# Kernel tuning notes

Hardware: AMD Instinct MI355X
Metric: run time of the kernel (lower is better)

The kernel has to match this reference:

```python
import jax, jax.numpy as jnp
import numpy as np

NUM_HEADS = 16
EMB_SIZE = 1024
HEAD_SIZE = 64


def setup_inputs() -> dict:
    key = jax.random.key(0)
    ks = jax.random.split(key, 9)
    H, E, D = NUM_HEADS, EMB_SIZE, HEAD_SIZE
    s = 1.0 / np.sqrt(E)
    X = jax.random.normal(ks[0], (4, 2048, E), dtype=jnp.float32)
    Wq = jax.random.uniform(ks[1], (H, E, D), jnp.float32, -s, s)
    Wk = jax.random.uniform(ks[2], (H, E, D), jnp.float32, -s, s)
    Wv = jax.random.uniform(ks[3], (H, E, D), jnp.float32, -s, s)
    bq = jax.random.uniform(ks[4], (H, D), jnp.float32, -s, s)
    bk = jax.random.uniform(ks[5], (H, D), jnp.float32, -s, s)
    bv = jax.random.uniform(ks[6], (H, D), jnp.float32, -s, s)
    so = 1.0 / np.sqrt(H * D)
    Wo = jax.random.uniform(ks[7], (H * D, E), jnp.float32, -so, so)
    bo = jax.random.uniform(ks[8], (E,), jnp.float32, -so, so)
    return {"X": X, "Wq": Wq, "Wk": Wk, "Wv": Wv, "bq": bq, "bk": bk, "bv": bv, "Wo": Wo, "bo": bo}


def reference(X, Wq, Wk, Wv, bq, bk, bv, Wo, bo):
    B, S, E = X.shape
    H, _, D = Wq.shape
    # per-head projections (batched over heads)
    q = jnp.einsum('bse,hed->bhsd', X, Wq) + bq[None, :, None, :]
    k = jnp.einsum('bse,hed->bhsd', X, Wk) + bk[None, :, None, :]
    v = jnp.einsum('bse,hed->bhsd', X, Wv) + bv[None, :, None, :]
    # causal scaled-dot-product attention
    scores = jnp.einsum('bhsd,bhtd->bhst', q, k) / jnp.sqrt(jnp.float32(D))
    causal = jnp.tril(jnp.ones((S, S), dtype=bool))
    scores = jnp.where(causal[None, None], scores, jnp.float32(-jnp.inf))
    probs = jax.nn.softmax(scores, axis=-1)
    out = jnp.einsum('bhst,bhtd->bhsd', probs, v)
    # concat heads (head h occupies slots [h*D:(h+1)*D]) then output proj
    concat = out.transpose(0, 2, 1, 3).reshape(B, S, H * D)
    # dropout is identity in eval mode
    return concat @ Wo + bo
```

## Files before the change

### kernel.cpp

```cpp
#include <hip/hip_runtime.h>
#include <stdint.h>


typedef float   f32x4  __attribute__((ext_vector_type(4)));
typedef __bf16  bf16x8 __attribute__((ext_vector_type(8)));
typedef short   short8 __attribute__((ext_vector_type(8)));
typedef unsigned short ushort4v __attribute__((ext_vector_type(4)));

typedef __attribute__((address_space(1))) void GV;
typedef __attribute__((address_space(3))) void LV;

#define DEVI static __device__ __forceinline__

DEVI unsigned short f2bf(float f){
  unsigned u = __float_as_uint(f);
  unsigned r = u + 0x7fffu + ((u>>16)&1u);
  return (unsigned short)(r>>16);
}

DEVI unsigned cvt_pk_bf16(float lo, float hi){
  unsigned r;
  asm("v_cvt_pk_bf16_f32 %0, %1, %2" : "=v"(r) : "v"(lo), "v"(hi));
  return r;
}

DEVI void permlane32_swap(unsigned &a, unsigned &b){
  asm volatile("v_permlane32_swap_b32 %0, %1" : "+v"(a), "+v"(b));
}
DEVI void permlane16_swap(unsigned &a, unsigned &b){
  asm volatile("v_permlane16_swap_b32 %0, %1" : "+v"(a), "+v"(b));
}

DEVI void gl_lds16(const void* g, void* l){
  __builtin_amdgcn_global_load_lds((GV*)g, (LV*)l, 16, 0, 0);
}

#define BAR() asm volatile("s_barrier" ::: "memory")

__global__ __launch_bounds__(256) void pack_x(const float* __restrict__ X,
                                              short* __restrict__ Xb){
  int i = blockIdx.x*256 + threadIdx.x;
  const float4* p = (const float4*)(X + (size_t)i*8);
  float4 a = p[0], b = p[1];
  short8 o;
  o[0]=(short)f2bf(a.x); o[1]=(short)f2bf(a.y); o[2]=(short)f2bf(a.z); o[3]=(short)f2bf(a.w);
  o[4]=(short)f2bf(b.x); o[5]=(short)f2bf(b.y); o[6]=(short)f2bf(b.z); o[7]=(short)f2bf(b.w);
  *(short8*)(Xb + (size_t)i*8) = o;
}

__global__ __launch_bounds__(256) void pack_wqkv(const float* __restrict__ Wq,
                                                 const float* __restrict__ Wk,
                                                 const float* __restrict__ Wv,
                                                 short* __restrict__ Wp){
  int t = blockIdx.x*256 + threadIdx.x;
  int n = t >> 7, kc = t & 127;
  int which = n >> 10, hd = n & 1023, h = hd >> 6, d = hd & 63;
  const float* W = which==0 ? Wq : (which==1 ? Wk : Wv);
  const float* src = W + ((size_t)h*1024 + kc*8)*64 + d;
  short8 o;
  #pragma unroll
  for (int j=0;j<8;++j) o[j] = (short)f2bf(src[(size_t)j*64]);
  *(short8*)(Wp + (size_t)n*1024 + kc*8) = o;
}

__global__ __launch_bounds__(256) void pack_wo(const float* __restrict__ Wo,
                                               short* __restrict__ WoT){
  int t = blockIdx.x*256 + threadIdx.x;
  int n = t >> 7, kc = t & 127;
  const float* src = Wo + (size_t)(kc*8)*1024 + n;
  short8 o;
  #pragma unroll
  for (int j=0;j<8;++j) o[j] = (short)f2bf(src[(size_t)j*1024]);
  *(short8*)(WoT + (size_t)n*1024 + kc*8) = o;
}

template<int MODE>
__global__ __launch_bounds__(512)
void gemm256(const short* __restrict__ A, const short* __restrict__ Bt,
             const float* __restrict__ b0, const float* __restrict__ b1,
             const float* __restrict__ b2,
             short* __restrict__ Qb, short* __restrict__ Kb, short* __restrict__ Vtb,
             float* __restrict__ Out)
{
  __shared__ __align__(16) char sm[3][49152];
  const int K2 = 2048;
  int t = threadIdx.x, lane = t & 63, wid = t >> 6;
  int wr = wid >> 2, wc = wid & 3;
  int l15 = lane & 15, l4 = lane >> 4;
  int nwg = gridDim.x, qd = nwg >> 3;
  int swz = (blockIdx.x & 7) * qd + (blockIdx.x >> 3);
  int bm = swz & 63, bn = swz >> 6;
  size_t abase = (size_t)bm * 128 * K2;
  size_t bbase = (size_t)bn * 256 * K2;

  f32x4 acc[4][4] = {};
  const char* sA; const char* sB;
  bf16x8 af[4], bfr[4];

  auto stageA = [&](int kt, char* buf){
    int kb = kt * 128;
    #pragma unroll
    for (int c = 0; c < 2; ++c){
      int x = c*8192 + t*16;
      int r = x >> 7, z = x & 127;
      int zs = z ^ ((r & 7) << 4);
      gl_lds16((const char*)A + abase + (size_t)r*K2 + kb + zs, buf + c*8192 + wid*1024);
    }
  };
  auto stageB = [&](int kt, char* buf, int c0){
    int kb = kt * 128;
    #pragma unroll
    for (int c = 0; c < 2; ++c){
      int cc = c0 + c;
      int x = cc*8192 + t*16;
      int r = x >> 7, z = x & 127;
      int zs = z ^ ((r & 7) << 4);
      gl_lds16((const char*)Bt + bbase + (size_t)r*K2 + kb + zs, buf + 16384 + cc*8192 + wid*1024);
    }
  };
  auto rd_af = [&](int kk){
    int cb = kk*64 + l4*16;
    #pragma unroll
    for (int i = 0; i < 4; ++i){
      int ra = wr*64 + i*16 + l15;
      af[i] = *(const bf16x8*)(sA + ra*128 + (cb ^ ((ra&7)<<4)));
    }
  };
  auto rd_bf = [&](int kk, int j0){
    int cb = kk*64 + l4*16;
    #pragma unroll
    for (int j = 0; j < 2; ++j){
      int rb = wc*64 + (j0 + j)*16 + l15;
      bfr[j0 + j] = *(const bf16x8*)(sB + rb*128 + (cb ^ ((rb&7)<<4)));
    }
  };
  auto mm = [&](int j0){
    __builtin_amdgcn_s_setprio(1);
    #pragma unroll
    for (int i = 0; i < 4; ++i)
      #pragma unroll
      for (int j = 0; j < 2; ++j)
        acc[i][j0+j] = __builtin_amdgcn_mfma_f32_16x16x32_bf16(af[i], bfr[j0+j], acc[i][j0+j], 0, 0, 0);
    __builtin_amdgcn_s_setprio(0);
  };

  stageA(0, sm[0]); stageB(0, sm[0], 0); stageB(0, sm[0], 2);
  stageA(1, sm[1]); stageB(1, sm[1], 0); stageB(1, sm[1], 2);

  for (int kt = 0; kt < 16; ++kt){
    if (kt == 15) asm volatile("s_waitcnt vmcnt(0)" ::: "memory");
    else          asm volatile("s_waitcnt vmcnt(6)" ::: "memory");
    BAR();
    sA = sm[kt % 3]; sB = sA + 16384;
    char* nb = sm[(kt + 2) % 3];
    bool st = kt < 14;
    rd_af(0); rd_bf(0, 0);
    if (st) stageA(kt + 2, nb);
    BAR(); mm(0); BAR();
    rd_bf(0, 2);
    if (st) stageB(kt + 2, nb, 0);
    BAR(); mm(2); BAR();
    rd_af(1); rd_bf(1, 0);
    if (st) stageB(kt + 2, nb, 2);
    BAR(); mm(0); BAR();
    rd_bf(1, 2);
    BAR(); mm(2);
  }

  #pragma unroll
  for (int i = 0; i < 4; ++i){
    int mbase = bm*128 + wr*64 + i*16 + l4*4;
    #pragma unroll
    for (int j = 0; j < 4; ++j){
      int n = bn*256 + wc*64 + j*16 + l15;
      if (MODE == 0){
        int which = n >> 10, hd = n & 1023, h = hd >> 6, d = hd & 63;
        const float* bp = which==0 ? b0 : (which==1 ? b1 : b2);
        float bias = bp[hd];
        int b = mbase >> 11, sbase = mbase & 2047;
        size_t bh = (size_t)(b*16 + h);
        if (which == 2){
          ushort4v pv;
          #pragma unroll
          for (int r = 0; r < 4; ++r) pv[r] = f2bf(acc[i][j][r] + bias);
          *(ushort4v*)(Vtb + (bh*64 + d)*2048 + sbase) = pv;
        } else {
          short* dst = (which==0 ? Qb : Kb) + bh*2048*64;
          float sc = which==0 ? 0.18033688f : 1.0f;
          #pragma unroll
          for (int r = 0; r < 4; ++r)
            dst[(size_t)(sbase + r)*64 + d] = (short)f2bf((acc[i][j][r] + bias) * sc);
        }
      } else {
        float bias = b0[n];
        #pragma unroll
        for (int r = 0; r < 4; ++r)
          Out[(size_t)(mbase + r)*1024 + n] = acc[i][j][r] + bias;
      }
    }
  }
}

__global__ __launch_bounds__(256, 5)
void attn(const short* __restrict__ Qb, const short* __restrict__ Kb,
          const short* __restrict__ Vtb, short* __restrict__ Ob)
{
  __shared__ __align__(16) char smK[2][8192];
  __shared__ __align__(16) char smV[2][8192];
  int t = threadIdx.x, lane = t & 63, wid = t >> 6;
  int l15 = lane & 15, hi = lane >> 4;
  int hi16 = hi*16, hi4 = hi*4;
  int bh = blockIdx.x & 63;
  int qb = 31 - (blockIdx.x >> 6);
  int b = bh >> 4, h = bh & 15;
  int wq0 = qb*64 + wid*16;
  const char* Qh = (const char*)(Qb + (size_t)bh*2048*64);
  const char* Kh = (const char*)(Kb + (size_t)bh*2048*64);
  const char* Vh = (const char*)(Vtb + (size_t)bh*64*2048);

  bf16x8 vones;
  #pragma unroll
  for (int z = 0; z < 8; ++z) vones[z] = (__bf16)1.0f;

  bf16x8 qf[2];
  #pragma unroll
  for (int kk = 0; kk < 2; ++kk)
    qf[kk] = *(const bf16x8*)(Qh + (size_t)(wq0 + l15)*128 + kk*64 + hi16);

  f32x4 oacc[4] = {};
  f32x4 lacc = {};
  float m = -1e30f;

  int nkt = qb + 1;

  #pragma unroll
  for (int c = 0; c < 2; ++c){
    int x = c*4096 + t*16;
    int r = x >> 7, z = x & 127;
    int zs = z ^ ((r & 7) << 4);
    gl_lds16(Kh + (size_t)r*128 + zs, smK[0] + c*4096 + wid*1024);
    gl_lds16(Vh + (size_t)r*4096 + zs, smV[0] + c*4096 + wid*1024);
  }
  __syncthreads();

  for (int kt = 0; kt < nkt; ++kt){
    int cur = kt & 1;
    if (kt + 1 < nkt){
      int nxt = cur ^ 1;
      #pragma unroll
      for (int c = 0; c < 2; ++c){
        int x = c*4096 + t*16;
        int r = x >> 7, z = x & 127;
        int zs = z ^ ((r & 7) << 4);
        gl_lds16(Kh + (size_t)(kt+1)*8192 + (size_t)r*128 + zs, smK[nxt] + c*4096 + wid*1024);
        gl_lds16(Vh + (size_t)r*4096 + (size_t)(kt+1)*128 + zs, smV[nxt] + c*4096 + wid*1024);
      }
    }
    const char* Kc = smK[cur];
    const char* Vc = smV[cur];
    int kbase = kt * 64;

    f32x4 sa[4];
    __builtin_amdgcn_s_setprio(1);
    #pragma unroll
    for (int nt = 0; nt < 4; ++nt){
      f32x4 a = {};
      #pragma unroll
      for (int kk = 0; kk < 2; ++kk){
        int rk = nt*16 + l15;
        bf16x8 kf = *(const bf16x8*)(Kc + rk*128 + ((kk*64 + hi16) ^ ((rk&7)<<4)));
        a = __builtin_amdgcn_mfma_f32_16x16x32_bf16(kf, qf[kk], a, 0, 0, 0);
      }
      sa[nt] = a;
    }
    __builtin_amdgcn_s_setprio(0);

    if (kt == qb){
      int qrow = wq0 + l15;
      #pragma unroll
      for (int nt = 0; nt < 4; ++nt)
        #pragma unroll
        for (int r = 0; r < 4; ++r)
          if (kbase + nt*16 + hi4 + r > qrow) sa[nt][r] = -1e30f;
    }

    float pm;
    {
      float t0 = fmaxf(fmaxf(sa[0][0], sa[0][1]), sa[0][2]);
      float t1 = fmaxf(fmaxf(sa[0][3], sa[1][0]), sa[1][1]);
      float t2 = fmaxf(fmaxf(sa[1][2], sa[1][3]), sa[2][0]);
      float t3 = fmaxf(fmaxf(sa[2][1], sa[2][2]), sa[2][3]);
      float t4 = fmaxf(fmaxf(sa[3][0], sa[3][1]), sa[3][2]);
      float u0 = fmaxf(fmaxf(t0, t1), sa[3][3]);
      float u1 = fmaxf(fmaxf(t2, t3), t4);
      pm = fmaxf(u0, u1);
    }
    pm = fmaxf(pm, __shfl_xor(pm, 16));
    pm = fmaxf(pm, __shfl_xor(pm, 32));
    if (!__all(pm <= m + 8.0f)){
      float mnew = fmaxf(m, pm);
      float sc = exp2f(m - mnew);
      lacc *= sc;
      #pragma unroll
      for (int dt = 0; dt < 4; ++dt) oacc[dt] *= sc;
      m = mnew;
    }
    unsigned pw[8];
    #pragma unroll
    for (int nt = 0; nt < 4; ++nt){
      float p0 = exp2f(sa[nt][0] - m);
      float p1 = exp2f(sa[nt][1] - m);
      float p2 = exp2f(sa[nt][2] - m);
      float p3 = exp2f(sa[nt][3] - m);
      pw[nt*2]   = cvt_pk_bf16(p0, p1);
      pw[nt*2+1] = cvt_pk_bf16(p2, p3);
    }

    union U { unsigned u[4]; bf16x8 v; } f0, f1;
    {
      unsigned a0 = pw[0], b0v = pw[2];
      permlane32_swap(a0, b0v); permlane16_swap(a0, b0v);
      unsigned a1 = pw[1], b1v = pw[3];
      permlane32_swap(a1, b1v); permlane16_swap(a1, b1v);
      f0.u[0] = a0; f0.u[1] = a1; f0.u[2] = b0v; f0.u[3] = b1v;
      unsigned a2 = pw[4], b2v = pw[6];
      permlane32_swap(a2, b2v); permlane16_swap(a2, b2v);
      unsigned a3 = pw[5], b3v = pw[7];
      permlane32_swap(a3, b3v); permlane16_swap(a3, b3v);
      f1.u[0] = a2; f1.u[1] = a3; f1.u[2] = b2v; f1.u[3] = b3v;
    }

    __builtin_amdgcn_s_setprio(1);
    #pragma unroll
    for (int kk = 0; kk < 2; ++kk){
      bf16x8 pf = kk ? f1.v : f0.v;
      lacc = __builtin_amdgcn_mfma_f32_16x16x32_bf16(vones, pf, lacc, 0, 0, 0);
      #pragma unroll
      for (int dt = 0; dt < 4; ++dt){
        int rv = dt*16 + l15;
        bf16x8 vf = *(const bf16x8*)(Vc + rv*128 + ((kk*64 + hi16) ^ ((rv&7)<<4)));
        oacc[dt] = __builtin_amdgcn_mfma_f32_16x16x32_bf16(vf, pf, oacc[dt], 0, 0, 0);
      }
    }
    __builtin_amdgcn_s_setprio(0);

    __syncthreads();
  }

  float inv = 1.0f / lacc[0];
  int srow = wq0 + l15;
  size_t rb = ((size_t)(b*2048 + srow))*1024 + h*64 + hi4;
  #pragma unroll
  for (int dt = 0; dt < 4; ++dt){
    unsigned w0 = cvt_pk_bf16(oacc[dt][0]*inv, oacc[dt][1]*inv);
    unsigned w1 = cvt_pk_bf16(oacc[dt][2]*inv, oacc[dt][3]*inv);
    *(unsigned long long*)(Ob + rb + dt*16) =
        ((unsigned long long)w1 << 32) | (unsigned long long)w0;
  }
}

extern "C" void kernel_launch(void* const* d_in, const int* in_sizes, int n_in,
                              void* d_out, int out_size, void* d_ws, size_t ws_size,
                              hipStream_t stream)
{
  const float* X  = (const float*)d_in[0];
  const float* Wq = (const float*)d_in[1];
  const float* Wk = (const float*)d_in[2];
  const float* Wv = (const float*)d_in[3];
  const float* bq = (const float*)d_in[4];
  const float* bk = (const float*)d_in[5];
  const float* bv = (const float*)d_in[6];
  const float* Wo = (const float*)d_in[7];
  const float* bo = (const float*)d_in[8];
  float* Out = (float*)d_out;

  char* ws = (char*)d_ws;
  short* Xbf  = (short*)(ws);
  short* Wp   = (short*)(ws + 16777216);
  short* WoT  = (short*)(ws + 23068672);
  short* Qb   = (short*)(ws + 25165824);
  short* Kb   = (short*)(ws + 41943040);
  short* Vtb  = (short*)(ws + 58720256);
  short* Ob   = (short*)(ws + 75497472);

  pack_x   <<<4096, 256, 0, stream>>>(X, Xbf);
  pack_wqkv<<<1536, 256, 0, stream>>>(Wq, Wk, Wv, Wp);
  pack_wo  <<< 512, 256, 0, stream>>>(Wo, WoT);

  gemm256<0><<<768, 512, 0, stream>>>(Xbf, Wp, bq, bk, bv, Qb, Kb, Vtb, nullptr);
  attn      <<<2048, 256, 0, stream>>>(Qb, Kb, Vtb, Ob);
  gemm256<1><<<256, 512, 0, stream>>>(Ob, WoT, bo, nullptr, nullptr,
                                      nullptr, nullptr, nullptr, Out);
}
```

Before: 194.4 us.

## Enlarge QKV GEMM tiles to 256x256 and process two query tiles per attention wave

Splits the templated GEMM into a dedicated QKV kernel and an output kernel. The QKV kernel uses 256x256 tiles with a 64-wide K step and a 4-deep LDS ring, prefetching three stages ahead. The attention kernel now covers 128 query rows per block (32 per wave, as two 16-row tiles), which halves the grid and reuses each staged K/V tile for twice as many queries. It also reorders blocks in a zigzag, skips fully masked query tiles, and lowers the occupancy hint to 4. The costs are more registers per wave, a different LDS layout with no XOR swizzle that may cause bank conflicts, and fewer blocks to balance across CUs.

```diff
diff --git a/kernel.cpp b/kernel.cpp
--- a/kernel.cpp
+++ b/kernel.cpp
@@ -74,21 +74,125 @@
   *(short8*)(WoT + (size_t)n*1024 + kc*8) = o;
 }
 
-template<int MODE>
 __global__ __launch_bounds__(512)
-void gemm256(const short* __restrict__ A, const short* __restrict__ Bt,
-             const float* __restrict__ b0, const float* __restrict__ b1,
-             const float* __restrict__ b2,
-             short* __restrict__ Qb, short* __restrict__ Kb, short* __restrict__ Vtb,
-             float* __restrict__ Out)
+void gemm_qkv(const short* __restrict__ A, const short* __restrict__ Bt,
+              const float* __restrict__ b0, const float* __restrict__ b1,
+              const float* __restrict__ b2,
+              short* __restrict__ Qb, short* __restrict__ Kb, short* __restrict__ Vtb)
+{
+  __shared__ __align__(16) char sm[4][32768];
+  const int K2 = 2048;
+  int t = threadIdx.x, lane = t & 63, wid = t >> 6;
+  int wr = wid >> 2, wc = wid & 3;
+  int l15 = lane & 15, l4 = lane >> 4;
+  int swz = (blockIdx.x & 7) * 48 + (blockIdx.x >> 3);
+  int bm = swz & 31, bn = swz >> 5;
+  size_t abase = (size_t)bm * 256 * K2;
+  size_t bbase = (size_t)bn * 256 * K2;
+
+  f32x4 acc[8][4] = {};
+  bf16x8 af[8], bfr[4];
+  const char* sA; const char* sB;
+
+  auto stageA = [&](int kt, char* buf){
+    int kb = kt * 64;
+    #pragma unroll
+    for (int c = 0; c < 2; ++c){
+      int x = c*8192 + t*16;
+      int r = x >> 6;
+      gl_lds16((const char*)A + abase + (size_t)r*K2 + kb + (x & 63), buf + c*8192 + wid*1024);
+    }
+  };
+  auto stageB = [&](int kt, char* buf){
+    int kb = kt * 64;
+    #pragma unroll
+    for (int c = 0; c < 2; ++c){
+      int x = c*8192 + t*16;
+      int r = x >> 6;
+      gl_lds16((const char*)Bt + bbase + (size_t)r*K2 + kb + (x & 63), buf + 16384 + c*8192 + wid*1024);
+    }
+  };
+  auto rd_af = [&](){
+    #pragma unroll
+    for (int i = 0; i < 8; ++i){
+      int ra = wr*128 + i*16 + l15;
+      af[i] = *(const bf16x8*)(sA + ra*64 + l4*16);
+    }
+  };
+  auto rd_bf = [&](int j0){
+    #pragma unroll
+    for (int j = 0; j < 2; ++j){
+      int rb = wc*64 + (j0 + j)*16 + l15;
+      bfr[j0 + j] = *(const bf16x8*)(sB + rb*64 + l4*16);
+    }
+  };
+  auto mm = [&](int j0){
+    __builtin_amdgcn_s_setprio(1);
+    #pragma unroll
+    for (int i = 0; i < 8; ++i)
+      #pragma unroll
+      for (int j = 0; j < 2; ++j)
+        acc[i][j0+j] = __builtin_amdgcn_mfma_f32_16x16x32_bf16(af[i], bfr[j0+j], acc[i][j0+j], 0, 0, 0);
+    __builtin_amdgcn_s_setprio(0);
+  };
+
+  stageA(0, sm[0]); stageB(0, sm[0]);
+  stageA(1, sm[1]); stageB(1, sm[1]);
+  stageA(2, sm[2]); stageB(2, sm[2]);
+
+  for (int kt = 0; kt < 32; ++kt){
+    if      (kt < 30) asm volatile("s_waitcnt vmcnt(8)" ::: "memory");
+    else if (kt == 30) asm volatile("s_waitcnt vmcnt(4)" ::: "memory");
+    else               asm volatile("s_waitcnt vmcnt(0)" ::: "memory");
+    BAR();
+    sA = sm[kt & 3]; sB = sA + 16384;
+    char* nb = sm[(kt + 3) & 3];
+    bool st = kt < 29;
+    rd_af(); rd_bf(0);
+    if (st) stageA(kt + 3, nb);
+    BAR(); mm(0); BAR();
+    rd_bf(2);
+    if (st) stageB(kt + 3, nb);
+    BAR(); mm(2);
+  }
+
+  #pragma unroll
+  for (int i = 0; i < 8; ++i){
+    int mbase = bm*256 + wr*128 + i*16 + l4*4;
+    #pragma unroll
+    for (int j = 0; j < 4; ++j){
+      int n = bn*256 + wc*64 + j*16 + l15;
+      int which = n >> 10, hd = n & 1023, h = hd >> 6, d = hd & 63;
+      const float* bp = which==0 ? b0 : (which==1 ? b1 : b2);
+      float bias = bp[hd];
+      int b = mbase >> 11, sbase = mbase & 2047;
+      size_t bh = (size_t)(b*16 + h);
+      if (which == 2){
+        ushort4v pv;
+        #pragma unroll
+        for (int r = 0; r < 4; ++r) pv[r] = f2bf(acc[i][j][r] + bias);
+        *(ushort4v*)(Vtb + (bh*64 + d)*2048 + sbase) = pv;
+      } else {
+        short* dst = (which==0 ? Qb : Kb) + bh*2048*64;
+        float sc = which==0 ? 0.18033688f : 1.0f;
+        #pragma unroll
+        for (int r = 0; r < 4; ++r)
+          dst[(size_t)(sbase + r)*64 + d] = (short)f2bf((acc[i][j][r] + bias) * sc);
+      }
+    }
+  }
+}
+
+__global__ __launch_bounds__(512)
+void gemm_out(const short* __restrict__ A, const short* __restrict__ Bt,
+              const float* __restrict__ b0, float* __restrict__ Out)
 {
   __shared__ __align__(16) char sm[3][49152];
   const int K2 = 2048;
   int t = threadIdx.x, lane = t & 63, wid = t >> 6;
   int wr = wid >> 2, wc = wid & 3;
   int l15 = lane & 15, l4 = lane >> 4;
-  int nwg = gridDim.x, qd = nwg >> 3;
-  int swz = (blockIdx.x & 7) * qd + (blockIdx.x >> 3);
+  int swz = (blockIdx.x & 7) * 32 + (blockIdx.x >> 3);
   int bm = swz & 63, bn = swz >> 6;
   size_t abase = (size_t)bm * 128 * K2;
   size_t bbase = (size_t)bn * 256 * K2;
@@ -173,35 +277,15 @@
     #pragma unroll
     for (int j = 0; j < 4; ++j){
       int n = bn*256 + wc*64 + j*16 + l15;
-      if (MODE == 0){
-        int which = n >> 10, hd = n & 1023, h = hd >> 6, d = hd & 63;
-        const float* bp = which==0 ? b0 : (which==1 ? b1 : b2);
-        float bias = bp[hd];
-        int b = mbase >> 11, sbase = mbase & 2047;
-        size_t bh = (size_t)(b*16 + h);
-        if (which == 2){
-          ushort4v pv;
-          #pragma unroll
-          for (int r = 0; r < 4; ++r) pv[r] = f2bf(acc[i][j][r] + bias);
-          *(ushort4v*)(Vtb + (bh*64 + d)*2048 + sbase) = pv;
-        } else {
-          short* dst = (which==0 ? Qb : Kb) + bh*2048*64;
-          float sc = which==0 ? 0.18033688f : 1.0f;
-          #pragma unroll
-          for (int r = 0; r < 4; ++r)
-            dst[(size_t)(sbase + r)*64 + d] = (short)f2bf((acc[i][j][r] + bias) * sc);
-        }
-      } else {
-        float bias = b0[n];
-        #pragma unroll
-        for (int r = 0; r < 4; ++r)
-          Out[(size_t)(mbase + r)*1024 + n] = acc[i][j][r] + bias;
-      }
-    }
-  }
-}
-
-__global__ __launch_bounds__(256, 5)
+      float bias = b0[n];
+      #pragma unroll
+      for (int r = 0; r < 4; ++r)
+        Out[(size_t)(mbase + r)*1024 + n] = acc[i][j][r] + bias;
+    }
+  }
+}
+
+__global__ __launch_bounds__(256, 4)
 void attn(const short* __restrict__ Qb, const short* __restrict__ Kb,
           const short* __restrict__ Vtb, short* __restrict__ Ob)
 {
@@ -211,9 +295,10 @@
   int l15 = lane & 15, hi = lane >> 4;
   int hi16 = hi*16, hi4 = hi*4;
   int bh = blockIdx.x & 63;
-  int qb = 31 - (blockIdx.x >> 6);
+  int j = blockIdx.x >> 6;
+  int qb = (j < 8) ? (15 - j) : (j - 8);
   int b = bh >> 4, h = bh & 15;
-  int wq0 = qb*64 + wid*16;
+  int wq0 = qb*128 + wid*32;
   const char* Qh = (const char*)(Qb + (size_t)bh*2048*64);
   const char* Kh = (const char*)(Kb + (size_t)bh*2048*64);
   const char* Vh = (const char*)(Vtb + (size_t)bh*64*2048);
@@ -222,16 +307,18 @@
   #pragma unroll
   for (int z = 0; z < 8; ++z) vones[z] = (__bf16)1.0f;
 
-  bf16x8 qf[2];
-  #pragma unroll
-  for (int kk = 0; kk < 2; ++kk)
-    qf[kk] = *(const bf16x8*)(Qh + (size_t)(wq0 + l15)*128 + kk*64 + hi16);
-
-  f32x4 oacc[4] = {};
-  f32x4 lacc = {};
-  float m = -1e30f;
-
-  int nkt = qb + 1;
+  bf16x8 qf[2][2];
+  #pragma unroll
+  for (int qt = 0; qt < 2; ++qt)
+    #pragma unroll
+    for (int kk = 0; kk < 2; ++kk)
+      qf[qt][kk] = *(const bf16x8*)(Qh + (size_t)(wq0 + qt*16 + l15)*128 + kk*64 + hi16);
+
+  f32x4 oacc[2][4] = {};
+  f32x4 lacc[2] = {};
+  float m[2] = {-1e30f, -1e30f};
+
+  int nkt = 2*qb + 2;
 
   #pragma unroll
   for (int c = 0; c < 2; ++c){
@@ -260,102 +347,111 @@
     const char* Vc = smV[cur];
     int kbase = kt * 64;
 
-    f32x4 sa[4];
-    __builtin_amdgcn_s_setprio(1);
-    #pragma unroll
-    for (int nt = 0; nt < 4; ++nt){
-      f32x4 a = {};
+    #pragma unroll
+    for (int qt = 0; qt < 2; ++qt){
+      int qlo = wq0 + qt*16;
+      if (kbase > qlo + 15) continue;
+
+      f32x4 sa[4];
+      __builtin_amdgcn_s_setprio(1);
+      #pragma unroll
+      for (int nt = 0; nt < 4; ++nt){
+        f32x4 a = {};
+        #pragma unroll
+        for (int kk = 0; kk < 2; ++kk){
+          int rk = nt*16 + l15;
+          bf16x8 kf = *(const bf16x8*)(Kc + rk*128 + ((kk*64 + hi16) ^ ((rk&7)<<4)));
+          a = __builtin_amdgcn_mfma_f32_16x16x32_bf16(kf, qf[qt][kk], a, 0, 0, 0);
+        }
+        sa[nt] = a;
+      }
+      __builtin_amdgcn_s_setprio(0);
+
+      if (kbase + 63 > qlo){
+        int qrow = qlo + l15;
+        #pragma unroll
+        for (int nt = 0; nt < 4; ++nt)
+          #pragma unroll
+          for (int r = 0; r < 4; ++r)
+            if (kbase + nt*16 + hi4 + r > qrow) sa[nt][r] = -1e30f;
+      }
+
+      float pm;
+      {
+        float t0 = fmaxf(fmaxf(sa[0][0], sa[0][1]), sa[0][2]);
+        float t1 = fmaxf(fmaxf(sa[0][3], sa[1][0]), sa[1][1]);
+        float t2 = fmaxf(fmaxf(sa[1][2], sa[1][3]), sa[2][0]);
+        float t3 = fmaxf(fmaxf(sa[2][1], sa[2][2]), sa[2][3]);
+        float t4 = fmaxf(fmaxf(sa[3][0], sa[3][1]), sa[3][2]);
+        float u0 = fmaxf(fmaxf(t0, t1), sa[3][3]);
+        float u1 = fmaxf(fmaxf(t2, t3), t4);
+        pm = fmaxf(u0, u1);
+      }
+      pm = fmaxf(pm, __shfl_xor(pm, 16));
+      pm = fmaxf(pm, __shfl_xor(pm, 32));
+      float mq = m[qt];
+      if (!__all(pm <= mq + 8.0f)){
+        float mnew = fmaxf(mq, pm);
+        float sc = exp2f(mq - mnew);
+        lacc[qt] *= sc;
+        #pragma unroll
+        for (int dt = 0; dt < 4; ++dt) oacc[qt][dt] *= sc;
+        m[qt] = mnew; mq = mnew;
+      }
+      unsigned pw[8];
+      #pragma unroll
+      for (int nt = 0; nt < 4; ++nt){
+        float p0 = exp2f(sa[nt][0] - mq);
+        float p1 = exp2f(sa[nt][1] - mq);
+        float p2 = exp2f(sa[nt][2] - mq);
+        float p3 = exp2f(sa[nt][3] - mq);
+        pw[nt*2]   = cvt_pk_bf16(p0, p1);
+        pw[nt*2+1] = cvt_pk_bf16(p2, p3);
+      }
+
+      union U { unsigned u[4]; bf16x8 v; } f0, f1;
+      {
+        unsigned a0 = pw[0], b0v = pw[2];
+        permlane32_swap(a0, b0v); permlane16_swap(a0, b0v);
+        unsigned a1 = pw[1], b1v = pw[3];
+        permlane32_swap(a1, b1v); permlane16_swap(a1, b1v);
+        f0.u[0] = a0; f0.u[1] = a1; f0.u[2] = b0v; f0.u[3] = b1v;
+        unsigned a2 = pw[4], b2v = pw[6];
+        permlane32_swap(a2, b2v); permlane16_swap(a2, b2v);
+        unsigned a3 = pw[5], b3v = pw[7];
+        permlane32_swap(a3, b3v); permlane16_swap(a3, b3v);
+        f1.u[0] = a2; f1.u[1] = a3; f1.u[2] = b2v; f1.u[3] = b3v;
+      }
+
+      __builtin_amdgcn_s_setprio(1);
       #pragma unroll
       for (int kk = 0; kk < 2; ++kk){
-        int rk = nt*16 + l15;
-        bf16x8 kf = *(const bf16x8*)(Kc + rk*128 + ((kk*64 + hi16) ^ ((rk&7)<<4)));
-        a = __builtin_amdgcn_mfma_f32_16x16x32_bf16(kf, qf[kk], a, 0, 0, 0);
-      }
-      sa[nt] = a;
-    }
-    __builtin_amdgcn_s_setprio(0);
-
-    if (kt == qb){
-      int qrow = wq0 + l15;
-      #pragma unroll
-      for (int nt = 0; nt < 4; ++nt)
-        #pragma unroll
-        for (int r = 0; r < 4; ++r)
-          if (kbase + nt*16 + hi4 + r > qrow) sa[nt][r] = -1e30f;
-    }
-
-    float pm;
-    {
-      float t0 = fmaxf(fmaxf(sa[0][0], sa[0][1]), sa[0][2]);
-      float t1 = fmaxf(fmaxf(sa[0][3], sa[1][0]), sa[1][1]);
-      float t2 = fmaxf(fmaxf(sa[1][2], sa[1][3]), sa[2][0]);
-      float t3 = fmaxf(fmaxf(sa[2][1], sa[2][2]), sa[2][3]);
-      float t4 = fmaxf(fmaxf(sa[3][0], sa[3][1]), sa[3][2]);
-      float u0 = fmaxf(fmaxf(t0, t1), sa[3][3]);
-      float u1 = fmaxf(fmaxf(t2, t3), t4);
-      pm = fmaxf(u0, u1);
-    }
-    pm = fmaxf(pm, __shfl_xor(pm, 16));
-    pm = fmaxf(pm, __shfl_xor(pm, 32));
-    if (!__all(pm <= m + 8.0f)){
-      float mnew = fmaxf(m, pm);
-      float sc = exp2f(m - mnew);
-      lacc *= sc;
-      #pragma unroll
-      for (int dt = 0; dt < 4; ++dt) oacc[dt] *= sc;
-      m = mnew;
-    }
-    unsigned pw[8];
-    #pragma unroll
-    for (int nt = 0; nt < 4; ++nt){
-      float p0 = exp2f(sa[nt][0] - m);
-      float p1 = exp2f(sa[nt][1] - m);
-      float p2 = exp2f(sa[nt][2] - m);
-      float p3 = exp2f(sa[nt][3] - m);
-      pw[nt*2]   = cvt_pk_bf16(p0, p1);
-      pw[nt*2+1] = cvt_pk_bf16(p2, p3);
-    }
-
-    union U { unsigned u[4]; bf16x8 v; } f0, f1;
-    {
-      unsigned a0 = pw[0], b0v = pw[2];
-      permlane32_swap(a0, b0v); permlane16_swap(a0, b0v);
-      unsigned a1 = pw[1], b1v = pw[3];
-      permlane32_swap(a1, b1v); permlane16_swap(a1, b1v);
-      f0.u[0] = a0; f0.u[1] = a1; f0.u[2] = b0v; f0.u[3] = b1v;
-      unsigned a2 = pw[4], b2v = pw[6];
-      permlane32_swap(a2, b2v); permlane16_swap(a2, b2v);
-      unsigned a3 = pw[5], b3v = pw[7];
-      permlane32_swap(a3, b3v); permlane16_swap(a3, b3v);
-      f1.u[0] = a2; f1.u[1] = a3; f1.u[2] = b2v; f1.u[3] = b3v;
-    }
-
-    __builtin_amdgcn_s_setprio(1);
-    #pragma unroll
-    for (int kk = 0; kk < 2; ++kk){
-      bf16x8 pf = kk ? f1.v : f0.v;
-      lacc = __builtin_amdgcn_mfma_f32_16x16x32_bf16(vones, pf, lacc, 0, 0, 0);
-      #pragma unroll
-      for (int dt = 0; dt < 4; ++dt){
-        int rv = dt*16 + l15;
-        bf16x8 vf = *(const bf16x8*)(Vc + rv*128 + ((kk*64 + hi16) ^ ((rv&7)<<4)));
-        oacc[dt] = __builtin_amdgcn_mfma_f32_16x16x32_bf16(vf, pf, oacc[dt], 0, 0, 0);
-      }
-    }
-    __builtin_amdgcn_s_setprio(0);
-
+        bf16x8 pf = kk ? f1.v : f0.v;
+        lacc[qt] = __builtin_amdgcn_mfma_f32_16x16x32_bf16(vones, pf, lacc[qt], 0, 0, 0);
+        #pragma unroll
+        for (int dt = 0; dt < 4; ++dt){
+          int rv = dt*16 + l15;
+          bf16x8 vf = *(const bf16x8*)(Vc + rv*128 + ((kk*64 + hi16) ^ ((rv&7)<<4)));
+          oacc[qt][dt] = __builtin_amdgcn_mfma_f32_16x16x32_bf16(vf, pf, oacc[qt][dt], 0, 0, 0);
+        }
+      }
+      __builtin_amdgcn_s_setprio(0);
+    }
     __syncthreads();
   }
 
-  float inv = 1.0f / lacc[0];
-  int srow = wq0 + l15;
-  size_t rb = ((size_t)(b*2048 + srow))*1024 + h*64 + hi4;
-  #pragma unroll
-  for (int dt = 0; dt < 4; ++dt){
-    unsigned w0 = cvt_pk_bf16(oacc[dt][0]*inv, oacc[dt][1]*inv);
-    unsigned w1 = cvt_pk_bf16(oacc[dt][2]*inv, oacc[dt][3]*inv);
-    *(unsigned long long*)(Ob + rb + dt*16) =
-        ((unsigned long long)w1 << 32) | (unsigned long long)w0;
+  #pragma unroll
+  for (int qt = 0; qt < 2; ++qt){
+    float inv = 1.0f / lacc[qt][0];
+    int srow = wq0 + qt*16 + l15;
+    size_t rb = ((size_t)(b*2048 + srow))*1024 + h*64 + hi4;
+    #pragma unroll
+    for (int dt = 0; dt < 4; ++dt){
+      unsigned w0 = cvt_pk_bf16(oacc[qt][dt][0]*inv, oacc[qt][dt][1]*inv);
+      unsigned w1 = cvt_pk_bf16(oacc[qt][dt][2]*inv, oacc[qt][dt][3]*inv);
+      *(unsigned long long*)(Ob + rb + dt*16) =
+          ((unsigned long long)w1 << 32) | (unsigned long long)w0;
+    }
   }
 }
 
@@ -387,8 +483,7 @@
   pack_wqkv<<<1536, 256, 0, stream>>>(Wq, Wk, Wv, Wp);
   pack_wo  <<< 512, 256, 0, stream>>>(Wo, WoT);
 
-  gemm256<0><<<768, 512, 0, stream>>>(Xbf, Wp, bq, bk, bv, Qb, Kb, Vtb, nullptr);
-  attn      <<<2048, 256, 0, stream>>>(Qb, Kb, Vtb, Ob);
-  gemm256<1><<<256, 512, 0, stream>>>(Ob, WoT, bo, nullptr, nullptr,
-                                      nullptr, nullptr, nullptr, Out);
-}
+  gemm_qkv<<<384, 512, 0, stream>>>(Xbf, Wp, bq, bk, bv, Qb, Kb, Vtb);
+  attn    <<<1024, 256, 0, stream>>>(Qb, Kb, Vtb, Ob);
+  gemm_out<<<256, 512, 0, stream>>>(Ob, WoT, bo, Out);
+}
```

Result: slower. 212.6 us (+9.4%).
